# Kernel optimization log

Hardware: AMD Instinct MI355X
Metric: run time of the kernel (lower is better)

Reference implementation:

```python
import jax, jax.numpy as jnp
from jax import lax
import numpy as np

B, CIN, L = 16, 512, 1024
COUT, K = 1024, 5          # conv out channels (GLU halves to 512), kernel size
DW = 512                    # word_feat == attn_channels == img_conv channels
HW = 196                    # 14*14 image feature locations


def setup_inputs() -> dict:
    key = jax.random.key(0)
    ks = jax.random.split(key, 8)
    s = 0.02
    return {
        "x": jax.random.normal(ks[0], (B, CIN, L), jnp.float32),
        "word_embed": jax.random.normal(ks[1], (B, L, DW), jnp.float32),
        "img_conv": jax.random.normal(ks[2], (B, DW, 14, 14), jnp.float32),
        "prev_attn": jnp.zeros((B, L, HW), jnp.float32),  # passed through, unused
        "conv_v": jax.random.normal(ks[3], (COUT, CIN, K), jnp.float32) * s,
        "conv_g": jnp.ones((COUT,), jnp.float32),
        "conv_b": jnp.zeros((COUT,), jnp.float32),
        "fc1_w": jax.random.normal(ks[4], (DW, DW), jnp.float32) * s,
        "fc1_b": jnp.zeros((DW,), jnp.float32),
        "fc2_w": jax.random.normal(ks[5], (DW, DW), jnp.float32) * s,
        "fc2_b": jnp.zeros((DW,), jnp.float32),
    }


def reference(x, word_embed, img_conv, prev_attn,
              conv_v, conv_g, conv_b, fc1_w, fc1_b, fc2_w, fc2_b):
    k = conv_v.shape[-1]
    # weight norm (PyTorch default dim=0): w = g * v / ||v||_{(in,k)}
    v_norm = jnp.sqrt(jnp.sum(conv_v * conv_v, axis=(1, 2), keepdims=True))
    w = (conv_g[:, None, None] / v_norm) * conv_v
    # Conv1d, padding=k-1 on both sides -> length L + k - 1 after ConvS2S trim
    y = lax.conv_general_dilated(x, w, window_strides=(1,),
                                 padding=[(k - 1, k - 1)],
                                 dimension_numbers=("NCH", "OIH", "NCH"))
    y = y + conv_b[None, :, None]
    # dropout is identity in eval mode
    a, b = jnp.split(y, 2, axis=1)          # GLU over channel dim
    h = a * jax.nn.sigmoid(b)
    h = h[:, :, : -(k - 1)]                  # [B, DW, L]
    identity_attn = h
    # attn_fc1 on [B, L, DW] then add word embeddings
    q = jnp.einsum("bcl,ac->bla", h, fc1_w) + fc1_b + word_embed  # [B, L, DW]
    feat = img_conv.reshape(img_conv.shape[0], img_conv.shape[1], -1)  # [B, DW, HW]
    score = jnp.einsum("bla,bap->blp", q, feat)   # [B, L, HW]
    attn = jax.nn.softmax(score, axis=-1)         # softmax over image locations
    ctx = jnp.einsum("blp,bap->bla", attn, feat)  # [B, L, DW]
    o = jnp.einsum("bla,ca->blc", ctx, fc2_w) + fc2_b
    out = o.transpose(0, 2, 1) + identity_attn
    # identity.shape == out.shape (input_feat == output_feat/2) -> no downsample
    out = out + x
    return (out, word_embed, img_conv, attn)
```

## Files before the change

### kernel.cpp

```cpp
#include <hip/hip_runtime.h>
#include <math.h>

#define NB   16
#define NCIN 512
#define NL   1024
#define NCOUT 1024
#define NK   5
#define NDW  512
#define NHW  196
#define NP   208
#define NPK  224
#define NLG  1028

typedef unsigned short ushort_t;
typedef unsigned int uint_t;
typedef __attribute__((ext_vector_type(8))) short bf16x8;
typedef __attribute__((ext_vector_type(4))) float f32x4;

static __device__ __forceinline__ ushort_t f2bf(float f) {
  uint_t u = __builtin_bit_cast(uint_t, f);
  u += 0x7fff + ((u >> 16) & 1);
  return (ushort_t)(u >> 16);
}
static __device__ __forceinline__ float bf2f(ushort_t u) {
  uint_t v = ((uint_t)u) << 16;
  return __builtin_bit_cast(float, v);
}

#define BARM()    asm volatile("s_barrier" ::: "memory")
#define WAITVM8() asm volatile("s_waitcnt vmcnt(8)" ::: "memory")
#define WAITVM0() asm volatile("s_waitcnt vmcnt(0)" ::: "memory")

static __device__ __forceinline__ void gld16(const ushort_t* g, ushort_t* l) {
  __builtin_amdgcn_global_load_lds(
      (const __attribute__((address_space(1))) unsigned int*)g,
      (__attribute__((address_space(3))) unsigned int*)l, 16, 0, 0);
}

__global__ __launch_bounds__(256) void wnorm_kernel(
    const float* __restrict__ v, const float* __restrict__ g,
    ushort_t* __restrict__ wperm) {
  const int o = blockIdx.x;
  const float* vr = v + (size_t)o * (NCIN * NK);
  float s = 0.f;
  for (int j = threadIdx.x; j < NCIN * NK; j += 256) {
    float t = vr[j];
    s += t * t;
  }
  for (int off = 32; off; off >>= 1) s += __shfl_down(s, off, 64);
  __shared__ float red[4];
  __shared__ float scale_s;
  const int wid = threadIdx.x >> 6;
  if ((threadIdx.x & 63) == 0) red[wid] = s;
  __syncthreads();
  if (threadIdx.x == 0) {
    float tot = red[0] + red[1] + red[2] + red[3];
    scale_s = g[o] / sqrtf(tot);
  }
  __syncthreads();
  const float scale = scale_s;
  const int isB = (o >= NDW) ? 1 : 0;
  const int c = o - isB * NDW;
  const int j = (c >> 5) * 64 + isB * 32 + (c & 31);
#pragma unroll
  for (int dk = 0; dk < NK; ++dk) {
    for (int ci = threadIdx.x; ci < NCIN; ci += 256) {
      wperm[((size_t)dk * NCOUT + j) * NCIN + ci] = f2bf(vr[ci * NK + dk] * scale);
    }
  }
}

__global__ __launch_bounds__(256) void xpose_kernel(
    const float* __restrict__ x, ushort_t* __restrict__ xT) {
  const int b = blockIdx.z;
  const int ci0 = blockIdx.y * 64;
  const int l0 = blockIdx.x * 64;
  const int tid = threadIdx.x;
  __shared__ float t[64][65];
  const float* xb = x + ((size_t)b * NCIN + ci0) * NL + l0;
#pragma unroll
  for (int r = 0; r < 4; ++r) {
    int row = r * 16 + (tid >> 4);
    int col = (tid & 15) * 4;
    float4 v = *(const float4*)&xb[(size_t)row * NL + col];
    t[row][col + 0] = v.x; t[row][col + 1] = v.y;
    t[row][col + 2] = v.z; t[row][col + 3] = v.w;
  }
  __syncthreads();
  ushort_t* xo = xT + ((size_t)b * NLG + l0 + 4) * NCIN + ci0;
#pragma unroll
  for (int r = 0; r < 4; ++r) {
    int lrow = r * 16 + (tid >> 4);
    int cic = (tid & 15) * 4;
    ushort4 o4;
    o4.x = f2bf(t[cic + 0][lrow]);
    o4.y = f2bf(t[cic + 1][lrow]);
    o4.z = f2bf(t[cic + 2][lrow]);
    o4.w = f2bf(t[cic + 3][lrow]);
    *(ushort4*)&xo[(size_t)lrow * NCIN + cic] = o4;
  }
  if (blockIdx.x == 0) {
    for (int i = tid; i < 4 * 64; i += 256) {
      int rr = i >> 6, cc = i & 63;
      xT[((size_t)b * NLG + rr) * NCIN + ci0 + cc] = 0;
    }
  }
}

__global__ __launch_bounds__(256) void wcvt_kernel(
    const float* __restrict__ w1, const float* __restrict__ w2,
    ushort_t* __restrict__ w1bf, ushort_t* __restrict__ w2bf) {
  const int i = (blockIdx.x * 256 + threadIdx.x) * 4;
  {
    float4 v = *(const float4*)&w1[i];
    ushort4 o; o.x = f2bf(v.x); o.y = f2bf(v.y); o.z = f2bf(v.z); o.w = f2bf(v.w);
    *(ushort4*)&w1bf[i] = o;
  }
  {
    float4 v = *(const float4*)&w2[i];
    ushort4 o; o.x = f2bf(v.x); o.y = f2bf(v.y); o.z = f2bf(v.z); o.w = f2bf(v.w);
    *(ushort4*)&w2bf[i] = o;
  }
}

__global__ __launch_bounds__(256) void ftrans_kernel(
    const float* __restrict__ feat, ushort_t* __restrict__ fThi,
    ushort_t* __restrict__ fTlo, ushort_t* __restrict__ fbf) {
  const int b = blockIdx.y;
  const int a0 = blockIdx.x * 64;
  const int tid = threadIdx.x;
  __shared__ float t[64][200];

  const float* fb_ = feat + ((size_t)b * NDW + a0) * NHW;
#pragma unroll
  for (int pp = 0; pp < 16; ++pp) {
    int row = pp * 4 + (tid >> 6);
#pragma unroll
    for (int cc = 0; cc < 4; ++cc) {
      int col = cc * 64 + (tid & 63);
      if (col < NHW) t[row][col] = fb_[(size_t)row * NHW + col];
    }
  }
  __syncthreads();

  for (int pp = 0; pp < 13; ++pp) {
    int p = pp * 16 + (tid >> 4);
    int j = (tid & 15) * 4;
    ushort4 hi4, lo4;
#pragma unroll
    for (int k = 0; k < 4; ++k) {
      float v = (p < NHW) ? t[j + k][p] : 0.f;
      ushort_t h = f2bf(v);
      float lof = v - bf2f(h);
      ushort_t l = f2bf(lof);
      ((ushort_t*)&hi4)[k] = h;
      ((ushort_t*)&lo4)[k] = l;
    }
    size_t base = ((size_t)b * NP + p) * NDW + a0 + j;
    *(ushort4*)&fThi[base] = hi4;
    *(ushort4*)&fTlo[base] = lo4;
  }

#pragma unroll
  for (int cc = 0; cc < 4; ++cc) {
    int col = cc * 64 + (tid & 63);
    if (col < NPK) {
#pragma unroll
      for (int rr = 0; rr < 16; ++rr) {
        int al = rr * 4 + (tid >> 6);
        float v = (col < NHW) ? t[al][col] : 0.f;
        fbf[((size_t)b * NDW + a0 + al) * NPK + col] = f2bf(v);
      }
    }
  }
}

__global__ __launch_bounds__(512, 2) void conv_glu_mfma(
    const ushort_t* __restrict__ xT, const ushort_t* __restrict__ wperm,
    const float* __restrict__ conv_b, ushort_t* __restrict__ hbfT) {
  const int bb = blockIdx.x >> 2;
  const int l0 = (blockIdx.x & 3) * 256;
  const int by = blockIdx.y;
  const int tid = threadIdx.x;
  const int wid = tid >> 6;
  const int lane = tid & 63;
  const int wm = wid >> 2;
  const int wn = wid & 3;
  const int quad = lane >> 4;
  const int l16 = lane & 15;
  const int sw = (l16 & 7) << 3;
  const int csrc = ((lane & 7) ^ (lane >> 3)) << 3;

  __shared__ ushort_t sA[2][256][64];
  __shared__ ushort_t sB[2][256][64];

  f32x4 acc[8][4];
#pragma unroll
  for (int mt = 0; mt < 8; ++mt)
#pragma unroll
    for (int nt = 0; nt < 4; ++nt) acc[mt][nt] = (f32x4){0.f, 0.f, 0.f, 0.f};

  const ushort_t* gAbase = xT + (size_t)(bb * NLG + l0) * NCIN;
  const int r0 = wid * 8 + (lane >> 3);
  ushort_t* lA0 = &sA[0][0][0] + (wid * 64 + lane) * 8;
  ushort_t* lB0 = &sB[0][0][0] + (wid * 64 + lane) * 8;

  auto stage = [&](int tt, int s) {
    const int dk = tt >> 3;
    const int ci0 = (tt & 7) << 6;
    const ushort_t* gA = gAbase + (size_t)dk * NCIN + ci0 + csrc;
    const ushort_t* gB = wperm + ((size_t)dk * NCOUT + by * 256) * NCIN + ci0 + csrc;
    ushort_t* lA = lA0 + s * (256 * 64);
    ushort_t* lB = lB0 + s * (256 * 64);
#pragma unroll
    for (int c = 0; c < 4; ++c) {
      gld16(gA + (size_t)(r0 + c * 64) * NCIN, lA + c * 4096);
      gld16(gB + (size_t)(r0 + c * 64) * NCIN, lB + c * 4096);
    }
  };

  stage(0, 0);
  stage(1, 1);
  WAITVM8();
  BARM();

  for (int t = 0; t < 40; ++t) {
    const int s = t & 1;
    bf16x8 af[4][2], bfr[4][2];

#pragma unroll
    for (int mt = 0; mt < 4; ++mt)
#pragma unroll
      for (int ks = 0; ks < 2; ++ks)
        af[mt][ks] = *(const bf16x8*)&sA[s][wm * 128 + mt * 16 + l16]
                                        [(ks * 32 + quad * 8) ^ sw];
#pragma unroll
    for (int nt = 0; nt < 2; ++nt)
#pragma unroll
      for (int ks = 0; ks < 2; ++ks)
        bfr[nt][ks] = *(const bf16x8*)&sB[s][wn * 64 + nt * 16 + l16]
                                         [(ks * 32 + quad * 8) ^ sw];
    BARM();
    __builtin_amdgcn_s_setprio(1);
#pragma unroll
    for (int ks = 0; ks < 2; ++ks)
#pragma unroll
      for (int nt = 0; nt < 2; ++nt)
#pragma unroll
        for (int mt = 0; mt < 4; ++mt)
          acc[mt][nt] = __builtin_amdgcn_mfma_f32_16x16x32_bf16(
              af[mt][ks], bfr[nt][ks], acc[mt][nt], 0, 0, 0);
    __builtin_amdgcn_s_setprio(0);
    BARM();

#pragma unroll
    for (int nt = 2; nt < 4; ++nt)
#pragma unroll
      for (int ks = 0; ks < 2; ++ks)
        bfr[nt][ks] = *(const bf16x8*)&sB[s][wn * 64 + nt * 16 + l16]
                                         [(ks * 32 + quad * 8) ^ sw];
    BARM();
    __builtin_amdgcn_s_setprio(1);
#pragma unroll
    for (int ks = 0; ks < 2; ++ks)
#pragma unroll
      for (int nt = 2; nt < 4; ++nt)
#pragma unroll
        for (int mt = 0; mt < 4; ++mt)
          acc[mt][nt] = __builtin_amdgcn_mfma_f32_16x16x32_bf16(
              af[mt][ks], bfr[nt][ks], acc[mt][nt], 0, 0, 0);
    __builtin_amdgcn_s_setprio(0);
    BARM();

#pragma unroll
    for (int mt = 0; mt < 4; ++mt)
#pragma unroll
      for (int ks = 0; ks < 2; ++ks)
        af[mt][ks] = *(const bf16x8*)&sA[s][wm * 128 + (4 + mt) * 16 + l16]
                                        [(ks * 32 + quad * 8) ^ sw];
    BARM();
    __builtin_amdgcn_s_setprio(1);
#pragma unroll
    for (int ks = 0; ks < 2; ++ks)
#pragma unroll
      for (int nt = 0; nt < 2; ++nt)
#pragma unroll
        for (int mt = 0; mt < 4; ++mt)
          acc[4 + mt][nt] = __builtin_amdgcn_mfma_f32_16x16x32_bf16(
              af[mt][ks], bfr[nt][ks], acc[4 + mt][nt], 0, 0, 0);
    __builtin_amdgcn_s_setprio(0);
    BARM();

    if (t < 38) stage(t + 2, s);
    __builtin_amdgcn_s_setprio(1);
#pragma unroll
    for (int ks = 0; ks < 2; ++ks)
#pragma unroll
      for (int nt = 2; nt < 4; ++nt)
#pragma unroll
        for (int mt = 0; mt < 4; ++mt)
          acc[4 + mt][nt] = __builtin_amdgcn_mfma_f32_16x16x32_bf16(
              af[mt][ks], bfr[nt][ks], acc[4 + mt][nt], 0, 0, 0);
    __builtin_amdgcn_s_setprio(0);

    if (t < 39) {
      if (t < 38) { WAITVM8(); } else { WAITVM0(); }
      BARM();
    }
  }

#pragma unroll
  for (int nt = 0; nt < 2; ++nt) {
    const int c = by * 128 + wn * 32 + nt * 16 + l16;
    const float ba = conv_b[c];
    const float bg = conv_b[c + NDW];
#pragma unroll
    for (int mt = 0; mt < 8; ++mt) {
      const int lg = l0 + wm * 128 + mt * 16 + quad * 4;
      ushort_t* ho = hbfT + ((size_t)bb * NL + lg) * NDW + c;
#pragma unroll
      for (int r = 0; r < 4; ++r) {
        float aa = acc[mt][nt][r] + ba;
        float gg = acc[mt][nt + 2][r] + bg;
        float hv = aa * (1.f / (1.f + __expf(-gg)));
        ho[(size_t)r * NDW] = f2bf(hv);
      }
    }
  }
}

__global__ __launch_bounds__(256, 2) void fc1_mfma(
    const ushort_t* __restrict__ hbfT, const ushort_t* __restrict__ w1bf,
    const float* __restrict__ fb, const float* __restrict__ we,
    ushort_t* __restrict__ qhi, ushort_t* __restrict__ qlo) {
  const int b  = blockIdx.z;
  const int a0 = blockIdx.y * 128;
  const int l0 = blockIdx.x * 128;
  const int tid = threadIdx.x;
  const int wid = tid >> 6;
  const int lane = tid & 63;
  const int wl = wid & 1;
  const int wc = wid >> 1;
  const int quad = lane >> 4;
  const int l16 = lane & 15;

  __shared__ ushort_t la[128][72];
  __shared__ ushort_t lb[128][72];

  f32x4 acc[4][4];
#pragma unroll
  for (int mt = 0; mt < 4; ++mt)
#pragma unroll
    for (int nt = 0; nt < 4; ++nt) acc[mt][nt] = (f32x4){0.f, 0.f, 0.f, 0.f};

  const ushort_t* hb = hbfT + (size_t)b * NL * NDW;

  for (int c0 = 0; c0 < NDW; c0 += 64) {
    __syncthreads();
#pragma unroll
    for (int it = 0; it < 4; ++it) {
      int t = tid + it * 256;
      int r = t >> 3, seg = t & 7;
      *(uint4*)&la[r][seg * 8] = *(const uint4*)(hb + (size_t)(l0 + r) * NDW + c0 + seg * 8);
    }
#pragma unroll
    for (int it = 0; it < 4; ++it) {
      int t = tid + it * 256;
      int r = t >> 3, seg = t & 7;
      *(uint4*)&lb[r][seg * 8] = *(const uint4*)(w1bf + (size_t)(a0 + r) * NDW + c0 + seg * 8);
    }
    __syncthreads();
#pragma unroll
    for (int ks = 0; ks < 2; ++ks) {
      bf16x8 af[4];
#pragma unroll
      for (int mt = 0; mt < 4; ++mt)
        af[mt] = *(const bf16x8*)&la[wl * 64 + mt * 16 + l16][ks * 32 + quad * 8];
#pragma unroll
      for (int nt = 0; nt < 4; ++nt) {
        bf16x8 bf = *(const bf16x8*)&lb[wc * 64 + nt * 16 + l16][ks * 32 + quad * 8];
#pragma unroll
        for (int mt = 0; mt < 4; ++mt)
          acc[mt][nt] = __builtin_amdgcn_mfma_f32_16x16x32_bf16(af[mt], bf, acc[mt][nt], 0, 0, 0);
      }
    }
  }

#pragma unroll
  for (int nt = 0; nt < 4; ++nt) {
    const int a = a0 + wc * 64 + nt * 16 + l16;
    const float bias = fb[a];
#pragma unroll
    for (int mt = 0; mt < 4; ++mt) {
      const int l = l0 + wl * 64 + mt * 16 + quad * 4;
#pragma unroll
      for (int r = 0; r < 4; ++r) {
        size_t idx = ((size_t)b * NL + l + r) * NDW + a;
        float qv = acc[mt][nt][r] + bias + we[idx];
        ushort_t h = f2bf(qv);
        float lof = qv - bf2f(h);
        qhi[idx] = h;
        qlo[idx] = f2bf(lof);
      }
    }
  }
}

__global__ __launch_bounds__(256) void score_softmax(
    const ushort_t* __restrict__ qhi, const ushort_t* __restrict__ qlo,
    const ushort_t* __restrict__ fThi, const ushort_t* __restrict__ fTlo,
    float* __restrict__ out_attn) {
  const int b  = blockIdx.y;
  const int l0 = blockIdx.x * 64;
  const int tid = threadIdx.x;
  const int wid = tid >> 6;
  const int lane = tid & 63;
  const int quad = lane >> 4;
  const int l16 = lane & 15;

  __shared__ ushort_t qh[64][36], ql[64][36];
  __shared__ ushort_t fh[208][36], fl[208][36];

  f32x4 acc[13];
#pragma unroll
  for (int nt = 0; nt < 13; ++nt) acc[nt] = (f32x4){0.f, 0.f, 0.f, 0.f};

  for (int kc = 0; kc < 16; ++kc) {
    const int a0 = kc * 32;
    __syncthreads();
    {
      int r = tid >> 2, seg = tid & 3;
      size_t src = ((size_t)b * NL + l0 + r) * NDW + a0 + seg * 8;
      *(uint4*)&qh[r][seg * 8] = *(const uint4*)(qhi + src);
      *(uint4*)&ql[r][seg * 8] = *(const uint4*)(qlo + src);
#pragma unroll
      for (int it = 0; it < 4; ++it) {
        int row = it * 64 + (tid >> 2);
        if (row < NP) {
          size_t fsrc = ((size_t)b * NP + row) * NDW + a0 + seg * 8;
          *(uint4*)&fh[row][seg * 8] = *(const uint4*)(fThi + fsrc);
          *(uint4*)&fl[row][seg * 8] = *(const uint4*)(fTlo + fsrc);
        }
      }
    }
    __syncthreads();
    bf16x8 ah = *(const bf16x8*)&qh[wid * 16 + l16][quad * 8];
    bf16x8 al = *(const bf16x8*)&ql[wid * 16 + l16][quad * 8];
#pragma unroll
    for (int nt = 0; nt < 13; ++nt) {
      bf16x8 bh = *(const bf16x8*)&fh[nt * 16 + l16][quad * 8];
      bf16x8 bl = *(const bf16x8*)&fl[nt * 16 + l16][quad * 8];
      acc[nt] = __builtin_amdgcn_mfma_f32_16x16x32_bf16(ah, bh, acc[nt], 0, 0, 0);
      acc[nt] = __builtin_amdgcn_mfma_f32_16x16x32_bf16(al, bh, acc[nt], 0, 0, 0);
      acc[nt] = __builtin_amdgcn_mfma_f32_16x16x32_bf16(ah, bl, acc[nt], 0, 0, 0);
    }
  }

  const bool v12 = (l16 < 4);
#pragma unroll
  for (int r = 0; r < 4; ++r) {
    float mx = -1e30f;
#pragma unroll
    for (int nt = 0; nt < 12; ++nt) mx = fmaxf(mx, acc[nt][r]);
    if (v12) mx = fmaxf(mx, acc[12][r]);
#pragma unroll
    for (int off = 1; off < 16; off <<= 1) mx = fmaxf(mx, __shfl_xor(mx, off, 16));
    float ex[13];
    float sum = 0.f;
#pragma unroll
    for (int nt = 0; nt < 12; ++nt) { ex[nt] = __expf(acc[nt][r] - mx); sum += ex[nt]; }
    ex[12] = v12 ? __expf(acc[12][r] - mx) : 0.f;
    sum += ex[12];
#pragma unroll
    for (int off = 1; off < 16; off <<= 1) sum += __shfl_xor(sum, off, 16);
    const float inv = 1.f / sum;
    const int l = l0 + wid * 16 + quad * 4 + r;
    float* ao = out_attn + ((size_t)b * NL + l) * NHW;
#pragma unroll
    for (int nt = 0; nt < 13; ++nt) {
      int p = nt * 16 + l16;
      if (p < NHW) ao[p] = ex[nt] * inv;
    }
  }
}

__global__ __launch_bounds__(256, 2) void ctx_mfma(
    const float* __restrict__ attn, const ushort_t* __restrict__ fbf,
    ushort_t* __restrict__ ctx_bf) {
  const int b  = blockIdx.z;
  const int a0 = blockIdx.y * 128;
  const int l0 = blockIdx.x * 128;
  const int tid = threadIdx.x;
  const int wid = tid >> 6;
  const int lane = tid & 63;
  const int wl = wid & 1;
  const int wc = wid >> 1;
  const int quad = lane >> 4;
  const int l16 = lane & 15;

  __shared__ ushort_t la[128][36];
  __shared__ ushort_t lb[128][36];

  f32x4 acc[4][4];
#pragma unroll
  for (int mt = 0; mt < 4; ++mt)
#pragma unroll
    for (int nt = 0; nt < 4; ++nt) acc[mt][nt] = (f32x4){0.f, 0.f, 0.f, 0.f};

  for (int kc = 0; kc < 7; ++kc) {
    const int p0 = kc * 32;
    __syncthreads();
#pragma unroll
    for (int it = 0; it < 2; ++it) {
      int r = it * 64 + (tid >> 2), seg = tid & 3;
      int pb = p0 + seg * 8;
      const float* src = attn + ((size_t)b * NL + l0 + r) * NHW + pb;
      ushort4 o[2];
      if (pb + 7 < NHW) {
        float4 v0 = *(const float4*)src;
        float4 v1 = *(const float4*)(src + 4);
        o[0].x = f2bf(v0.x); o[0].y = f2bf(v0.y); o[0].z = f2bf(v0.z); o[0].w = f2bf(v0.w);
        o[1].x = f2bf(v1.x); o[1].y = f2bf(v1.y); o[1].z = f2bf(v1.z); o[1].w = f2bf(v1.w);
      } else {
#pragma unroll
        for (int k = 0; k < 8; ++k) {
          float v = (pb + k < NHW) ? src[k] : 0.f;
          ((ushort_t*)o)[k] = f2bf(v);
        }
      }
      *(uint4*)&la[r][seg * 8] = *(uint4*)o;
      const ushort_t* fsrc = fbf + ((size_t)b * NDW + a0 + r) * NPK + pb;
      *(uint4*)&lb[r][seg * 8] = *(const uint4*)fsrc;
    }
    __syncthreads();
    bf16x8 af[4];
#pragma unroll
    for (int mt = 0; mt < 4; ++mt)
      af[mt] = *(const bf16x8*)&la[wl * 64 + mt * 16 + l16][quad * 8];
#pragma unroll
    for (int nt = 0; nt < 4; ++nt) {
      bf16x8 bf = *(const bf16x8*)&lb[wc * 64 + nt * 16 + l16][quad * 8];
#pragma unroll
      for (int mt = 0; mt < 4; ++mt)
        acc[mt][nt] = __builtin_amdgcn_mfma_f32_16x16x32_bf16(af[mt], bf, acc[mt][nt], 0, 0, 0);
    }
  }

#pragma unroll
  for (int nt = 0; nt < 4; ++nt) {
    const int a = a0 + wc * 64 + nt * 16 + l16;
#pragma unroll
    for (int mt = 0; mt < 4; ++mt) {
      const int l = l0 + wl * 64 + mt * 16 + quad * 4;
#pragma unroll
      for (int r = 0; r < 4; ++r)
        ctx_bf[((size_t)b * NL + l + r) * NDW + a] = f2bf(acc[mt][nt][r]);
    }
  }
}

__global__ __launch_bounds__(256, 2) void fc2_mfma(
    const ushort_t* __restrict__ w2bf, const ushort_t* __restrict__ ctx_bf,
    const float* __restrict__ fb2, const ushort_t* __restrict__ hbfT,
    const float* __restrict__ x, float* __restrict__ out0) {
  const int b  = blockIdx.z;
  const int c0 = blockIdx.y * 128;
  const int l0 = blockIdx.x * 128;
  const int tid = threadIdx.x;
  const int wid = tid >> 6;
  const int lane = tid & 63;
  const int wl = wid & 1;
  const int wc = wid >> 1;
  const int quad = lane >> 4;
  const int l16 = lane & 15;

  __shared__ ushort_t la[128][72];
  __shared__ ushort_t lb[128][72];

  f32x4 acc[4][4];
#pragma unroll
  for (int mt = 0; mt < 4; ++mt)
#pragma unroll
    for (int nt = 0; nt < 4; ++nt) acc[mt][nt] = (f32x4){0.f, 0.f, 0.f, 0.f};

  for (int a0 = 0; a0 < NDW; a0 += 64) {
    __syncthreads();
#pragma unroll
    for (int it = 0; it < 4; ++it) {
      int t = tid + it * 256;
      int r = t >> 3, seg = t & 7;
      *(uint4*)&la[r][seg * 8] = *(const uint4*)(w2bf + (size_t)(c0 + r) * NDW + a0 + seg * 8);
    }
#pragma unroll
    for (int it = 0; it < 4; ++it) {
      int t = tid + it * 256;
      int r = t >> 3, seg = t & 7;
      *(uint4*)&lb[r][seg * 8] =
          *(const uint4*)(ctx_bf + ((size_t)b * NL + l0 + r) * NDW + a0 + seg * 8);
    }
    __syncthreads();
#pragma unroll
    for (int ks = 0; ks < 2; ++ks) {
      bf16x8 af[4];
#pragma unroll
      for (int mt = 0; mt < 4; ++mt)
        af[mt] = *(const bf16x8*)&la[wl * 64 + mt * 16 + l16][ks * 32 + quad * 8];
#pragma unroll
      for (int nt = 0; nt < 4; ++nt) {
        bf16x8 bf = *(const bf16x8*)&lb[wc * 64 + nt * 16 + l16][ks * 32 + quad * 8];
#pragma unroll
        for (int mt = 0; mt < 4; ++mt)
          acc[mt][nt] = __builtin_amdgcn_mfma_f32_16x16x32_bf16(af[mt], bf, acc[mt][nt], 0, 0, 0);
      }
    }
  }

#pragma unroll
  for (int mt = 0; mt < 4; ++mt) {
    const int cb = c0 + wl * 64 + mt * 16 + quad * 4;
    float4 bias4 = *(const float4*)&fb2[cb];
#pragma unroll
    for (int nt = 0; nt < 4; ++nt) {
      const int l = l0 + wc * 64 + nt * 16 + l16;
      ushort4 h4 = *(const ushort4*)&hbfT[((size_t)b * NL + l) * NDW + cb];
      const float bias[4] = {bias4.x, bias4.y, bias4.z, bias4.w};
      const ushort_t hs[4] = {h4.x, h4.y, h4.z, h4.w};
#pragma unroll
      for (int r = 0; r < 4; ++r) {
        size_t idx = ((size_t)b * NDW + cb + r) * NL + l;
        out0[idx] = acc[mt][nt][r] + bias[r] + bf2f(hs[r]) + x[idx];
      }
    }
  }
}

extern "C" void kernel_launch(void* const* d_in, const int* in_sizes, int n_in,
                              void* d_out, int out_size, void* d_ws, size_t ws_size,
                              hipStream_t stream) {
  const float* x      = (const float*)d_in[0];
  const float* we     = (const float*)d_in[1];
  const float* img    = (const float*)d_in[2];
  const float* conv_v = (const float*)d_in[4];
  const float* conv_g = (const float*)d_in[5];
  const float* conv_b = (const float*)d_in[6];
  const float* fc1_w  = (const float*)d_in[7];
  const float* fc1_b  = (const float*)d_in[8];
  const float* fc2_w  = (const float*)d_in[9];
  const float* fc2_b  = (const float*)d_in[10];

  float* out0     = (float*)d_out;
  float* out_we   = out0 + 8388608;
  float* out_img  = out_we + 8388608;
  float* out_attn = out_img + 1605632;

  ushort_t* wsu = (ushort_t*)d_ws;
  ushort_t* qhi   = wsu;
  ushort_t* qlo   = wsu + 8388608;
  ushort_t* wperm = wsu;
  ushort_t* xT    = wsu + 2621440;
  ushort_t* ctx_b = wsu;
  ushort_t* hbfT  = wsu + 16777216;
  ushort_t* w1bf  = wsu + 25165824;
  ushort_t* w2bf  = wsu + 25165824 + 262144;
  ushort_t* fThi  = wsu + 25690112;
  ushort_t* fTlo  = wsu + 27394048;
  ushort_t* fbf   = wsu + 29097984;

  wnorm_kernel<<<dim3(NCOUT), 256, 0, stream>>>(conv_v, conv_g, wperm);
  xpose_kernel<<<dim3(16, 8, NB), 256, 0, stream>>>(x, xT);
  wcvt_kernel<<<dim3(256), 256, 0, stream>>>(fc1_w, fc2_w, w1bf, w2bf);
  ftrans_kernel<<<dim3(8, NB), 256, 0, stream>>>(img, fThi, fTlo, fbf);

  conv_glu_mfma<<<dim3(64, 4), 512, 0, stream>>>(xT, wperm, conv_b, hbfT);
  fc1_mfma<<<dim3(8, 4, NB), 256, 0, stream>>>(hbfT, w1bf, fc1_b, we, qhi, qlo);
  score_softmax<<<dim3(16, NB), 256, 0, stream>>>(qhi, qlo, fThi, fTlo, out_attn);
  ctx_mfma<<<dim3(8, 4, NB), 256, 0, stream>>>(out_attn, fbf, ctx_b);
  fc2_mfma<<<dim3(8, 4, NB), 256, 0, stream>>>(w2bf, ctx_b, fc2_b, hbfT, x, out0);

  hipMemcpyAsync(out_we, we, (size_t)8388608 * sizeof(float),
                 hipMemcpyDeviceToDevice, stream);
  hipMemcpyAsync(out_img, img, (size_t)1605632 * sizeof(float),
                 hipMemcpyDeviceToDevice, stream);
}
```

Measured before the change: 410.4 us.

## Fuse fc1, score-softmax and ctx GEMM into one attention kernel

Merges the fc1 projection, score+softmax and attention-context GEMM into a single kernel per 64-row tile. The h tile is staged in LDS, q is computed per 32-column chunk in LDS, and the softmax probabilities stay in LDS for the ctx GEMM. This removes the q hi/lo round-trip through global memory, the re-read of attn as fp32, and two launches. In exchange it uses a large LDS footprint at one block per CU with only 256 blocks, which lowers occupancy and parallelism, and it reloads the fc1 weight rows in every block.

```diff
diff --git a/kernel.cpp b/kernel.cpp
--- a/kernel.cpp
+++ b/kernel.cpp
@@ -329,87 +329,12 @@
   }
 }
 
-__global__ __launch_bounds__(256, 2) void fc1_mfma(
+__global__ __launch_bounds__(256, 1) void attn_fused(
     const ushort_t* __restrict__ hbfT, const ushort_t* __restrict__ w1bf,
-    const float* __restrict__ fb, const float* __restrict__ we,
-    ushort_t* __restrict__ qhi, ushort_t* __restrict__ qlo) {
-  const int b  = blockIdx.z;
-  const int a0 = blockIdx.y * 128;
-  const int l0 = blockIdx.x * 128;
-  const int tid = threadIdx.x;
-  const int wid = tid >> 6;
-  const int lane = tid & 63;
-  const int wl = wid & 1;
-  const int wc = wid >> 1;
-  const int quad = lane >> 4;
-  const int l16 = lane & 15;
-
-  __shared__ ushort_t la[128][72];
-  __shared__ ushort_t lb[128][72];
-
-  f32x4 acc[4][4];
-#pragma unroll
-  for (int mt = 0; mt < 4; ++mt)
-#pragma unroll
-    for (int nt = 0; nt < 4; ++nt) acc[mt][nt] = (f32x4){0.f, 0.f, 0.f, 0.f};
-
-  const ushort_t* hb = hbfT + (size_t)b * NL * NDW;
-
-  for (int c0 = 0; c0 < NDW; c0 += 64) {
-    __syncthreads();
-#pragma unroll
-    for (int it = 0; it < 4; ++it) {
-      int t = tid + it * 256;
-      int r = t >> 3, seg = t & 7;
-      *(uint4*)&la[r][seg * 8] = *(const uint4*)(hb + (size_t)(l0 + r) * NDW + c0 + seg * 8);
-    }
-#pragma unroll
-    for (int it = 0; it < 4; ++it) {
-      int t = tid + it * 256;
-      int r = t >> 3, seg = t & 7;
-      *(uint4*)&lb[r][seg * 8] = *(const uint4*)(w1bf + (size_t)(a0 + r) * NDW + c0 + seg * 8);
-    }
-    __syncthreads();
-#pragma unroll
-    for (int ks = 0; ks < 2; ++ks) {
-      bf16x8 af[4];
-#pragma unroll
-      for (int mt = 0; mt < 4; ++mt)
-        af[mt] = *(const bf16x8*)&la[wl * 64 + mt * 16 + l16][ks * 32 + quad * 8];
-#pragma unroll
-      for (int nt = 0; nt < 4; ++nt) {
-        bf16x8 bf = *(const bf16x8*)&lb[wc * 64 + nt * 16 + l16][ks * 32 + quad * 8];
-#pragma unroll
-        for (int mt = 0; mt < 4; ++mt)
-          acc[mt][nt] = __builtin_amdgcn_mfma_f32_16x16x32_bf16(af[mt], bf, acc[mt][nt], 0, 0, 0);
-      }
-    }
-  }
-
-#pragma unroll
-  for (int nt = 0; nt < 4; ++nt) {
-    const int a = a0 + wc * 64 + nt * 16 + l16;
-    const float bias = fb[a];
-#pragma unroll
-    for (int mt = 0; mt < 4; ++mt) {
-      const int l = l0 + wl * 64 + mt * 16 + quad * 4;
-#pragma unroll
-      for (int r = 0; r < 4; ++r) {
-        size_t idx = ((size_t)b * NL + l + r) * NDW + a;
-        float qv = acc[mt][nt][r] + bias + we[idx];
-        ushort_t h = f2bf(qv);
-        float lof = qv - bf2f(h);
-        qhi[idx] = h;
-        qlo[idx] = f2bf(lof);
-      }
-    }
-  }
-}
-
-__global__ __launch_bounds__(256) void score_softmax(
-    const ushort_t* __restrict__ qhi, const ushort_t* __restrict__ qlo,
+    const float* __restrict__ fb1, const float* __restrict__ we,
     const ushort_t* __restrict__ fThi, const ushort_t* __restrict__ fTlo,
-    float* __restrict__ out_attn) {
+    const ushort_t* __restrict__ fbf, float* __restrict__ out_attn,
+    ushort_t* __restrict__ ctx_bf) {
   const int b  = blockIdx.y;
   const int l0 = blockIdx.x * 64;
   const int tid = threadIdx.x;
@@ -418,8 +343,23 @@
   const int quad = lane >> 4;
   const int l16 = lane & 15;
 
-  __shared__ ushort_t qh[64][36], ql[64][36];
-  __shared__ ushort_t fh[208][36], fl[208][36];
+  __shared__ ushort_t smem[69504];
+  ushort_t* hT = smem;
+  ushort_t* wS = smem + 33280;
+  ushort_t* qh = smem + 49920;
+  ushort_t* ql = smem + 52224;
+  ushort_t* fh = smem + 54528;
+  ushort_t* fl = smem + 62016;
+  ushort_t* pa = smem;
+  ushort_t* fb = smem + 14848;
+
+#pragma unroll
+  for (int it = 0; it < 16; ++it) {
+    int lin = tid + it * 256;
+    int r = lin >> 6, seg = lin & 63;
+    *(uint4*)&hT[r * 520 + seg * 8] =
+        *(const uint4*)(hbfT + ((size_t)b * NL + l0 + r) * NDW + seg * 8);
+  }
 
   f32x4 acc[13];
 #pragma unroll
@@ -430,26 +370,58 @@
     __syncthreads();
     {
       int r = tid >> 2, seg = tid & 3;
-      size_t src = ((size_t)b * NL + l0 + r) * NDW + a0 + seg * 8;
-      *(uint4*)&qh[r][seg * 8] = *(const uint4*)(qhi + src);
-      *(uint4*)&ql[r][seg * 8] = *(const uint4*)(qlo + src);
 #pragma unroll
       for (int it = 0; it < 4; ++it) {
-        int row = it * 64 + (tid >> 2);
+        int row = it * 64 + r;
         if (row < NP) {
           size_t fsrc = ((size_t)b * NP + row) * NDW + a0 + seg * 8;
-          *(uint4*)&fh[row][seg * 8] = *(const uint4*)(fThi + fsrc);
-          *(uint4*)&fl[row][seg * 8] = *(const uint4*)(fTlo + fsrc);
+          *(uint4*)&fh[row * 36 + seg * 8] = *(const uint4*)(fThi + fsrc);
+          *(uint4*)&fl[row * 36 + seg * 8] = *(const uint4*)(fTlo + fsrc);
         }
       }
+#pragma unroll
+      for (int it = 0; it < 8; ++it) {
+        int lin = tid + it * 256;
+        int rr = lin >> 6, ss = lin & 63;
+        *(uint4*)&wS[rr * 520 + ss * 8] =
+            *(const uint4*)(w1bf + (size_t)(a0 + rr) * NDW + ss * 8);
+      }
     }
     __syncthreads();
-    bf16x8 ah = *(const bf16x8*)&qh[wid * 16 + l16][quad * 8];
-    bf16x8 al = *(const bf16x8*)&ql[wid * 16 + l16][quad * 8];
+
+    f32x4 aq[2][2];
+    aq[0][0] = aq[0][1] = aq[1][0] = aq[1][1] = (f32x4){0.f, 0.f, 0.f, 0.f};
+#pragma unroll
+    for (int cs = 0; cs < 16; ++cs) {
+      bf16x8 af = *(const bf16x8*)&hT[(wid * 16 + l16) * 520 + cs * 32 + quad * 8];
+#pragma unroll
+      for (int nt = 0; nt < 2; ++nt) {
+        bf16x8 bw = *(const bf16x8*)&wS[(nt * 16 + l16) * 520 + cs * 32 + quad * 8];
+        aq[cs & 1][nt] = __builtin_amdgcn_mfma_f32_16x16x32_bf16(af, bw, aq[cs & 1][nt], 0, 0, 0);
+      }
+    }
+#pragma unroll
+    for (int nt = 0; nt < 2; ++nt) {
+      const int a = a0 + nt * 16 + l16;
+      const float bias = fb1[a];
+#pragma unroll
+      for (int r = 0; r < 4; ++r) {
+        const int l = l0 + wid * 16 + quad * 4 + r;
+        float qv = aq[0][nt][r] + aq[1][nt][r] + bias + we[((size_t)b * NL + l) * NDW + a];
+        ushort_t h = f2bf(qv);
+        const int row = wid * 16 + quad * 4 + r;
+        qh[row * 36 + nt * 16 + l16] = h;
+        ql[row * 36 + nt * 16 + l16] = f2bf(qv - bf2f(h));
+      }
+    }
+    __syncthreads();
+
+    bf16x8 ah = *(const bf16x8*)&qh[(wid * 16 + l16) * 36 + quad * 8];
+    bf16x8 al = *(const bf16x8*)&ql[(wid * 16 + l16) * 36 + quad * 8];
 #pragma unroll
     for (int nt = 0; nt < 13; ++nt) {
-      bf16x8 bh = *(const bf16x8*)&fh[nt * 16 + l16][quad * 8];
-      bf16x8 bl = *(const bf16x8*)&fl[nt * 16 + l16][quad * 8];
+      bf16x8 bh = *(const bf16x8*)&fh[(nt * 16 + l16) * 36 + quad * 8];
+      bf16x8 bl = *(const bf16x8*)&fl[(nt * 16 + l16) * 36 + quad * 8];
       acc[nt] = __builtin_amdgcn_mfma_f32_16x16x32_bf16(ah, bh, acc[nt], 0, 0, 0);
       acc[nt] = __builtin_amdgcn_mfma_f32_16x16x32_bf16(al, bh, acc[nt], 0, 0, 0);
       acc[nt] = __builtin_amdgcn_mfma_f32_16x16x32_bf16(ah, bl, acc[nt], 0, 0, 0);
@@ -478,83 +450,57 @@
     float* ao = out_attn + ((size_t)b * NL + l) * NHW;
 #pragma unroll
     for (int nt = 0; nt < 13; ++nt) {
+      float av = ex[nt] * inv;
+      acc[nt][r] = av;
       int p = nt * 16 + l16;
-      if (p < NHW) ao[p] = ex[nt] * inv;
-    }
-  }
-}
-
-__global__ __launch_bounds__(256, 2) void ctx_mfma(
-    const float* __restrict__ attn, const ushort_t* __restrict__ fbf,
-    ushort_t* __restrict__ ctx_bf) {
-  const int b  = blockIdx.z;
-  const int a0 = blockIdx.y * 128;
-  const int l0 = blockIdx.x * 128;
-  const int tid = threadIdx.x;
-  const int wid = tid >> 6;
-  const int lane = tid & 63;
-  const int wl = wid & 1;
-  const int wc = wid >> 1;
-  const int quad = lane >> 4;
-  const int l16 = lane & 15;
-
-  __shared__ ushort_t la[128][36];
-  __shared__ ushort_t lb[128][36];
-
-  f32x4 acc[4][4];
-#pragma unroll
-  for (int mt = 0; mt < 4; ++mt)
-#pragma unroll
-    for (int nt = 0; nt < 4; ++nt) acc[mt][nt] = (f32x4){0.f, 0.f, 0.f, 0.f};
-
-  for (int kc = 0; kc < 7; ++kc) {
-    const int p0 = kc * 32;
+      if (p < NHW) ao[p] = av;
+    }
+  }
+
+  __syncthreads();
+
+#pragma unroll
+  for (int r = 0; r < 4; ++r) {
+    const int row = wid * 16 + quad * 4 + r;
+#pragma unroll
+    for (int nt = 0; nt < 13; ++nt) {
+      int p = nt * 16 + l16;
+      pa[row * 232 + p] = (p < NHW) ? f2bf(acc[nt][r]) : (ushort_t)0;
+    }
+    pa[row * 232 + 208 + l16] = 0;
+  }
+
+  for (int ac = 0; ac < 8; ++ac) {
+    const int a0 = ac * 64;
     __syncthreads();
 #pragma unroll
-    for (int it = 0; it < 2; ++it) {
-      int r = it * 64 + (tid >> 2), seg = tid & 3;
-      int pb = p0 + seg * 8;
-      const float* src = attn + ((size_t)b * NL + l0 + r) * NHW + pb;
-      ushort4 o[2];
-      if (pb + 7 < NHW) {
-        float4 v0 = *(const float4*)src;
-        float4 v1 = *(const float4*)(src + 4);
-        o[0].x = f2bf(v0.x); o[0].y = f2bf(v0.y); o[0].z = f2bf(v0.z); o[0].w = f2bf(v0.w);
-        o[1].x = f2bf(v1.x); o[1].y = f2bf(v1.y); o[1].z = f2bf(v1.z); o[1].w = f2bf(v1.w);
-      } else {
-#pragma unroll
-        for (int k = 0; k < 8; ++k) {
-          float v = (pb + k < NHW) ? src[k] : 0.f;
-          ((ushort_t*)o)[k] = f2bf(v);
-        }
-      }
-      *(uint4*)&la[r][seg * 8] = *(uint4*)o;
-      const ushort_t* fsrc = fbf + ((size_t)b * NDW + a0 + r) * NPK + pb;
-      *(uint4*)&lb[r][seg * 8] = *(const uint4*)fsrc;
+    for (int it = 0; it < 7; ++it) {
+      int lin = tid + it * 256;
+      int rr = lin / 28, ss = lin % 28;
+      *(uint4*)&fb[rr * 232 + ss * 8] =
+          *(const uint4*)(fbf + ((size_t)b * NDW + a0 + rr) * NPK + ss * 8);
     }
     __syncthreads();
-    bf16x8 af[4];
-#pragma unroll
-    for (int mt = 0; mt < 4; ++mt)
-      af[mt] = *(const bf16x8*)&la[wl * 64 + mt * 16 + l16][quad * 8];
+    f32x4 ca[4];
+#pragma unroll
+    for (int nt = 0; nt < 4; ++nt) ca[nt] = (f32x4){0.f, 0.f, 0.f, 0.f};
+#pragma unroll
+    for (int ks = 0; ks < 7; ++ks) {
+      bf16x8 af = *(const bf16x8*)&pa[(wid * 16 + l16) * 232 + ks * 32 + quad * 8];
+#pragma unroll
+      for (int nt = 0; nt < 4; ++nt) {
+        bf16x8 bv = *(const bf16x8*)&fb[(nt * 16 + l16) * 232 + ks * 32 + quad * 8];
+        ca[nt] = __builtin_amdgcn_mfma_f32_16x16x32_bf16(af, bv, ca[nt], 0, 0, 0);
+      }
+    }
 #pragma unroll
     for (int nt = 0; nt < 4; ++nt) {
-      bf16x8 bf = *(const bf16x8*)&lb[wc * 64 + nt * 16 + l16][quad * 8];
-#pragma unroll
-      for (int mt = 0; mt < 4; ++mt)
-        acc[mt][nt] = __builtin_amdgcn_mfma_f32_16x16x32_bf16(af[mt], bf, acc[mt][nt], 0, 0, 0);
-    }
-  }
-
-#pragma unroll
-  for (int nt = 0; nt < 4; ++nt) {
-    const int a = a0 + wc * 64 + nt * 16 + l16;
-#pragma unroll
-    for (int mt = 0; mt < 4; ++mt) {
-      const int l = l0 + wl * 64 + mt * 16 + quad * 4;
-#pragma unroll
-      for (int r = 0; r < 4; ++r)
-        ctx_bf[((size_t)b * NL + l + r) * NDW + a] = f2bf(acc[mt][nt][r]);
+      const int a = a0 + nt * 16 + l16;
+#pragma unroll
+      for (int r = 0; r < 4; ++r) {
+        const int l = l0 + wid * 16 + quad * 4 + r;
+        ctx_bf[((size_t)b * NL + l) * NDW + a] = f2bf(ca[nt][r]);
+      }
     }
   }
 }
@@ -654,8 +600,6 @@
   float* out_attn = out_img + 1605632;
 
   ushort_t* wsu = (ushort_t*)d_ws;
-  ushort_t* qhi   = wsu;
-  ushort_t* qlo   = wsu + 8388608;
   ushort_t* wperm = wsu;
   ushort_t* xT    = wsu + 2621440;
   ushort_t* ctx_b = wsu;
@@ -672,9 +616,8 @@
   ftrans_kernel<<<dim3(8, NB), 256, 0, stream>>>(img, fThi, fTlo, fbf);
 
   conv_glu_mfma<<<dim3(64, 4), 512, 0, stream>>>(xT, wperm, conv_b, hbfT);
-  fc1_mfma<<<dim3(8, 4, NB), 256, 0, stream>>>(hbfT, w1bf, fc1_b, we, qhi, qlo);
-  score_softmax<<<dim3(16, NB), 256, 0, stream>>>(qhi, qlo, fThi, fTlo, out_attn);
-  ctx_mfma<<<dim3(8, 4, NB), 256, 0, stream>>>(out_attn, fbf, ctx_b);
+  attn_fused<<<dim3(16, NB), 256, 0, stream>>>(hbfT, w1bf, fc1_b, we,
+                                               fThi, fTlo, fbf, out_attn, ctx_b);
   fc2_mfma<<<dim3(8, 4, NB), 256, 0, stream>>>(w2bf, ctx_b, fc2_b, hbfT, x, out0);
 
   hipMemcpyAsync(out_we, we, (size_t)8388608 * sizeof(float),
```

Result: slower. 440.9 us (+7.4%).
